# Kernel tuning notes

Measured on AMD Instinct MI355X. Metric: run time of the kernel, lower is better.

Reference implementation:

```python
import jax, jax.numpy as jnp
import numpy as np


def setup_inputs() -> dict:
    key = jax.random.key(0)
    k1, k2 = jax.random.split(key)
    B, P, C, N = 32, 3, 512, 1024
    input_data1 = jax.random.normal(k1, (B, P, C, N), dtype=jnp.float32)
    input_data2 = jax.random.normal(k2, (B, P, C, N), dtype=jnp.float32)
    return {"input_data1": input_data1, "input_data2": input_data2}


def reference(input_data1, input_data2):
    # HorizontalComparisonModel.compare_algorithm_method4 (the only path used):
    # permute [B,P,C,N] -> [B,P,N,C], reshape to [B, P*N, C] pairs of C-dim vectors.
    B = input_data1.shape[0]
    x = jnp.transpose(input_data1, (0, 1, 3, 2)).reshape(B, -1, input_data1.shape[2])
    y = jnp.transpose(input_data2, (0, 1, 3, 2)).reshape(B, -1, input_data2.shape[2])
    d = x - y                                   # [B, pairs, C]
    l1 = jnp.sum(jnp.abs(d), axis=-1)           # temp31: L1 distance
    sq_l2 = jnp.sum(d * d, axis=-1)             # temp21: squared L2 distance
    # Original stacks [temp31, temp21, temp31] (L1 appears twice; cosine unused).
    out = jnp.stack([l1, sq_l2, l1], axis=-1)   # [B, pairs, 3]
    return out.reshape(B, -1)
```

## Files before the change

kernel.cpp:

```cpp
#include <hip/hip_runtime.h>

constexpr int B = 32, P = 3, C = 512, N = 1024;
constexpr int G = B * P;
constexpr int CSPLIT = 8;
constexpr int CCHUNK = C / CSPLIT;

__global__ __launch_bounds__(256) void dist_partial_kernel(
    const float* __restrict__ x1, const float* __restrict__ x2,
    float* __restrict__ out)
{
    const int g     = blockIdx.x / CSPLIT;
    const int chunk = blockIdx.x % CSPLIT;
    const int t     = threadIdx.x;

    const float4* a = (const float4*)(x1 + (size_t)g * C * N) + t;
    const float4* b = (const float4*)(x2 + (size_t)g * C * N) + t;
    const int c0 = chunk * CCHUNK;

    float4 l1 = make_float4(0.f, 0.f, 0.f, 0.f);
    float4 l2 = make_float4(0.f, 0.f, 0.f, 0.f);

    #pragma unroll 4
    for (int c = c0; c < c0 + CCHUNK; ++c) {
        const float4 av = a[(size_t)c * (N / 4)];
        const float4 bv = b[(size_t)c * (N / 4)];
        const float dx = av.x - bv.x;
        const float dy = av.y - bv.y;
        const float dz = av.z - bv.z;
        const float dw = av.w - bv.w;
        l1.x += fabsf(dx); l1.y += fabsf(dy); l1.z += fabsf(dz); l1.w += fabsf(dw);
        l2.x = fmaf(dx, dx, l2.x); l2.y = fmaf(dy, dy, l2.y);
        l2.z = fmaf(dz, dz, l2.z); l2.w = fmaf(dw, dw, l2.w);
    }

    const size_t obase = ((size_t)g * N + 4 * (size_t)t) * 3;
    const float l1v[4] = {l1.x, l1.y, l1.z, l1.w};
    const float l2v[4] = {l2.x, l2.y, l2.z, l2.w};
    #pragma unroll
    for (int i = 0; i < 4; ++i) {
        atomicAdd(&out[obase + 3 * i + 0], l1v[i]);
        atomicAdd(&out[obase + 3 * i + 1], l2v[i]);
        atomicAdd(&out[obase + 3 * i + 2], l1v[i]);
    }
}

extern "C" void kernel_launch(void* const* d_in, const int* in_sizes, int n_in,
                              void* d_out, int out_size, void* d_ws, size_t ws_size,
                              hipStream_t stream) {
    const float* x1 = (const float*)d_in[0];
    const float* x2 = (const float*)d_in[1];
    float* out = (float*)d_out;

    hipMemsetAsync(d_out, 0, (size_t)out_size * sizeof(float), stream);

    dist_partial_kernel<<<G * CSPLIT, 256, 0, stream>>>(x1, x2, out);
}
```

Before: 461.4 us.

## Replace atomic accumulation with workspace partials and combine kernel, deeper unroll

Doubles the channel split to launch more blocks and unrolls the inner loop to issue eight vector loads per iteration, raising memory-level parallelism. Per-chunk partial sums are written to a workspace and reduced by a second kernel instead of using a memset plus atomics into the output. This adds a kernel launch and roughly 12 MB of extra workspace traffic. The old atomic path is kept as a fallback when the workspace is too small.

```diff
diff --git a/kernel.cpp b/kernel.cpp
--- a/kernel.cpp
+++ b/kernel.cpp
@@ -2,37 +2,100 @@
 
 constexpr int B = 32, P = 3, C = 512, N = 1024;
 constexpr int G = B * P;
-constexpr int CSPLIT = 8;
+constexpr int CSPLIT = 16;
 constexpr int CCHUNK = C / CSPLIT;
+constexpr size_t WS_NEED = (size_t)CSPLIT * G * N * 2 * sizeof(float);
 
-__global__ __launch_bounds__(256) void dist_partial_kernel(
+__global__ __launch_bounds__(256) void dist_partial(
+    const float* __restrict__ x1, const float* __restrict__ x2,
+    float* __restrict__ ws)
+{
+    const int g     = blockIdx.x / CSPLIT;
+    const int chunk = blockIdx.x % CSPLIT;
+    const int t     = threadIdx.x;
+
+    const float4* pa = (const float4*)(x1 + (size_t)g * C * N)
+                       + (size_t)chunk * CCHUNK * (N / 4) + t;
+    const float4* pb = (const float4*)(x2 + (size_t)g * C * N)
+                       + (size_t)chunk * CCHUNK * (N / 4) + t;
+
+    float4 l1 = make_float4(0.f, 0.f, 0.f, 0.f);
+    float4 l2 = make_float4(0.f, 0.f, 0.f, 0.f);
+
+    #pragma unroll
+    for (int j = 0; j < CCHUNK; j += 4) {
+        const float4 a0 = pa[0 * (N / 4)];
+        const float4 a1 = pa[1 * (N / 4)];
+        const float4 a2 = pa[2 * (N / 4)];
+        const float4 a3 = pa[3 * (N / 4)];
+        const float4 b0 = pb[0 * (N / 4)];
+        const float4 b1 = pb[1 * (N / 4)];
+        const float4 b2 = pb[2 * (N / 4)];
+        const float4 b3 = pb[3 * (N / 4)];
+        pa += N;
+        pb += N;
+        float d;
+        d = a0.x - b0.x; l1.x += fabsf(d); l2.x = fmaf(d, d, l2.x);
+        d = a0.y - b0.y; l1.y += fabsf(d); l2.y = fmaf(d, d, l2.y);
+        d = a0.z - b0.z; l1.z += fabsf(d); l2.z = fmaf(d, d, l2.z);
+        d = a0.w - b0.w; l1.w += fabsf(d); l2.w = fmaf(d, d, l2.w);
+        d = a1.x - b1.x; l1.x += fabsf(d); l2.x = fmaf(d, d, l2.x);
+        d = a1.y - b1.y; l1.y += fabsf(d); l2.y = fmaf(d, d, l2.y);
+        d = a1.z - b1.z; l1.z += fabsf(d); l2.z = fmaf(d, d, l2.z);
+        d = a1.w - b1.w; l1.w += fabsf(d); l2.w = fmaf(d, d, l2.w);
+        d = a2.x - b2.x; l1.x += fabsf(d); l2.x = fmaf(d, d, l2.x);
+        d = a2.y - b2.y; l1.y += fabsf(d); l2.y = fmaf(d, d, l2.y);
+        d = a2.z - b2.z; l1.z += fabsf(d); l2.z = fmaf(d, d, l2.z);
+        d = a2.w - b2.w; l1.w += fabsf(d); l2.w = fmaf(d, d, l2.w);
+        d = a3.x - b3.x; l1.x += fabsf(d); l2.x = fmaf(d, d, l2.x);
+        d = a3.y - b3.y; l1.y += fabsf(d); l2.y = fmaf(d, d, l2.y);
+        d = a3.z - b3.z; l1.z += fabsf(d); l2.z = fmaf(d, d, l2.z);
+        d = a3.w - b3.w; l1.w += fabsf(d); l2.w = fmaf(d, d, l2.w);
+    }
+
+    float4* wout = (float4*)ws + ((size_t)(chunk * G + g) * N) / 2 + 2 * t;
+    wout[0] = make_float4(l1.x, l2.x, l1.y, l2.y);
+    wout[1] = make_float4(l1.z, l2.z, l1.w, l2.w);
+}
+
+__global__ __launch_bounds__(256) void dist_combine(
+    const float* __restrict__ ws, float* __restrict__ out)
+{
+    const int idx = blockIdx.x * 256 + threadIdx.x;
+    const float2* ws2 = (const float2*)ws;
+    float l1 = 0.f, l2 = 0.f;
+    #pragma unroll
+    for (int chunk = 0; chunk < CSPLIT; ++chunk) {
+        const float2 v = ws2[(size_t)chunk * G * N + idx];
+        l1 += v.x;
+        l2 += v.y;
+    }
+    out[3 * (size_t)idx + 0] = l1;
+    out[3 * (size_t)idx + 1] = l2;
+    out[3 * (size_t)idx + 2] = l1;
+}
+
+__global__ __launch_bounds__(256) void dist_atomic(
     const float* __restrict__ x1, const float* __restrict__ x2,
     float* __restrict__ out)
 {
     const int g     = blockIdx.x / CSPLIT;
     const int chunk = blockIdx.x % CSPLIT;
     const int t     = threadIdx.x;
-
     const float4* a = (const float4*)(x1 + (size_t)g * C * N) + t;
     const float4* b = (const float4*)(x2 + (size_t)g * C * N) + t;
     const int c0 = chunk * CCHUNK;
-
     float4 l1 = make_float4(0.f, 0.f, 0.f, 0.f);
     float4 l2 = make_float4(0.f, 0.f, 0.f, 0.f);
-
-    #pragma unroll 4
     for (int c = c0; c < c0 + CCHUNK; ++c) {
         const float4 av = a[(size_t)c * (N / 4)];
         const float4 bv = b[(size_t)c * (N / 4)];
-        const float dx = av.x - bv.x;
-        const float dy = av.y - bv.y;
-        const float dz = av.z - bv.z;
-        const float dw = av.w - bv.w;
-        l1.x += fabsf(dx); l1.y += fabsf(dy); l1.z += fabsf(dz); l1.w += fabsf(dw);
-        l2.x = fmaf(dx, dx, l2.x); l2.y = fmaf(dy, dy, l2.y);
-        l2.z = fmaf(dz, dz, l2.z); l2.w = fmaf(dw, dw, l2.w);
+        float d;
+        d = av.x - bv.x; l1.x += fabsf(d); l2.x = fmaf(d, d, l2.x);
+        d = av.y - bv.y; l1.y += fabsf(d); l2.y = fmaf(d, d, l2.y);
+        d = av.z - bv.z; l1.z += fabsf(d); l2.z = fmaf(d, d, l2.z);
+        d = av.w - bv.w; l1.w += fabsf(d); l2.w = fmaf(d, d, l2.w);
     }
-
     const size_t obase = ((size_t)g * N + 4 * (size_t)t) * 3;
     const float l1v[4] = {l1.x, l1.y, l1.z, l1.w};
     const float l2v[4] = {l2.x, l2.y, l2.z, l2.w};
@@ -51,7 +114,11 @@
     const float* x2 = (const float*)d_in[1];
     float* out = (float*)d_out;
 
-    hipMemsetAsync(d_out, 0, (size_t)out_size * sizeof(float), stream);
-
-    dist_partial_kernel<<<G * CSPLIT, 256, 0, stream>>>(x1, x2, out);
+    if (ws_size >= WS_NEED) {
+        dist_partial<<<G * CSPLIT, 256, 0, stream>>>(x1, x2, (float*)d_ws);
+        dist_combine<<<(G * N) / 256, 256, 0, stream>>>((const float*)d_ws, out);
+    } else {
+        hipMemsetAsync(d_out, 0, (size_t)out_size * sizeof(float), stream);
+        dist_atomic<<<G * CSPLIT, 256, 0, stream>>>(x1, x2, out);
+    }
 }
```

Result: faster. 392.6 us (-14.9%).
